# Kernel tuning notes

Measured on AMD Instinct MI355X. Metric: run time of the kernel, lower is better.

Reference implementation:

```python
import jax, jax.numpy as jnp
import numpy as np

N, D = 4096, 512
W_L2, W_TOPO = 1.0, 1.0
BIG = jnp.float32(1e30)


def setup_inputs() -> dict:
    key = jax.random.key(0)
    k1, k2 = jax.random.split(key)
    x_1 = jax.random.normal(k1, (N, D), dtype=jnp.float32)
    x_2 = jax.random.normal(k2, (N, D), dtype=jnp.float32)
    return {"x_1": x_1, "x_2": x_2}


def _pdist(x):
    # Euclidean pairwise distances [n, n]; diagonal set to BIG so it is never
    # selected as an MST edge and sqrt(0) never appears in the grad path.
    sq = jnp.sum(x * x, axis=1)
    d2 = sq[:, None] + sq[None, :] - 2.0 * (x @ x.T)
    d2 = jnp.maximum(d2, 1e-12)
    n = x.shape[0]
    d2 = jnp.where(jnp.eye(n, dtype=bool), BIG, d2)
    return jnp.sqrt(d2)


def _h0_deaths(dist):
    # H0 persistence of the Vietoris-Rips filtration == MST edge weights
    # (births are all 0). Prim's algorithm via lax.scan, O(n^2).
    n = dist.shape[0]
    in_tree0 = jnp.zeros(n, dtype=bool).at[0].set(True)

    def step(carry, _):
        min_dist, in_tree = carry  # min_dist[k] = min edge from tree to k
        md = jnp.where(in_tree, BIG, min_dist)
        j = jnp.argmin(md)
        w = md[j]  # weight of the MST edge added this step = an H0 death
        min_dist = jnp.minimum(min_dist, dist[j])
        in_tree = in_tree.at[j].set(True)
        return (min_dist, in_tree), w

    (_, _), deaths = jax.lax.scan(step, (dist[0], in_tree0), None, length=n - 1)
    return deaths  # [n-1]


def _wasserstein1(d1, d2):
    # 1-Wasserstein between two H0 diagrams {(0, death_i)} with L_inf ground
    # metric and diagonal projections allowed. Equal-cardinality diagrams on
    # the birth=0 axis: match sorted deaths, per-pair cost is the cheaper of
    # direct matching |a-b| or routing both points to the diagonal (a+b)/2.
    a = jnp.sort(d1)
    b = jnp.sort(d2)
    cost = jnp.minimum(jnp.abs(a - b), 0.5 * (a + b))
    return jnp.sum(cost)


def reference(x_1, x_2):
    representation_loss = jnp.mean((x_1 - x_2) ** 2)
    deaths_1 = _h0_deaths(_pdist(x_1))
    deaths_2 = _h0_deaths(_pdist(x_2))
    topological_loss = _wasserstein1(deaths_1, deaths_2)
    return W_L2 * representation_loss + W_TOPO * topological_loss
```

## Files before the change

kernel.cpp:

```cpp
#include <hip/hip_runtime.h>

#define N 4096
#define D 512
#define BIG 1e30f
#define CMAX 2048
#define CMAX2 1024
#define NW (N / 32)

typedef unsigned long long u64;
typedef unsigned short u16;
typedef _Float16 f16x8 __attribute__((ext_vector_type(8)));
typedef float floatx4 __attribute__((ext_vector_type(4)));

__global__ __launch_bounds__(256) void prep_kernel(const float* __restrict__ x1,
                                                   const float* __restrict__ x2,
                                                   u16* __restrict__ h1,
                                                   u16* __restrict__ h2,
                                                   float* __restrict__ sq,
                                                   float* __restrict__ accumArr,
                                                   int* __restrict__ comp,
                                                   u64* __restrict__ compBest,
                                                   int* __restrict__ comp_c,
                                                   int* __restrict__ doneFlag) {
    const int tid = blockIdx.x * 256 + threadIdx.x;
    if (tid < 2 * N) {
        comp[tid] = tid & (N - 1);
        compBest[tid] = ~0ull;
    }
    if (tid < 2 * CMAX) comp_c[tid] = tid & (CMAX - 1);
    if (tid == 0) doneFlag[0] = 0;

    const int wave = threadIdx.x >> 6, lane = threadIdx.x & 63;
    const int row = blockIdx.x * 4 + wave;
    const float4* r1 = (const float4*)(x1 + (size_t)row * D);
    const float4* r2 = (const float4*)(x2 + (size_t)row * D);
    float4 a0 = r1[lane * 2], a1 = r1[lane * 2 + 1];
    float4 b0 = r2[lane * 2], b1 = r2[lane * 2 + 1];
    ushort4* o1 = (ushort4*)(h1 + (size_t)row * D + lane * 8);
    ushort4* o2 = (ushort4*)(h2 + (size_t)row * D + lane * 8);
    o1[0] = make_ushort4(__builtin_bit_cast(u16, (_Float16)a0.x), __builtin_bit_cast(u16, (_Float16)a0.y),
                         __builtin_bit_cast(u16, (_Float16)a0.z), __builtin_bit_cast(u16, (_Float16)a0.w));
    o1[1] = make_ushort4(__builtin_bit_cast(u16, (_Float16)a1.x), __builtin_bit_cast(u16, (_Float16)a1.y),
                         __builtin_bit_cast(u16, (_Float16)a1.z), __builtin_bit_cast(u16, (_Float16)a1.w));
    o2[0] = make_ushort4(__builtin_bit_cast(u16, (_Float16)b0.x), __builtin_bit_cast(u16, (_Float16)b0.y),
                         __builtin_bit_cast(u16, (_Float16)b0.z), __builtin_bit_cast(u16, (_Float16)b0.w));
    o2[1] = make_ushort4(__builtin_bit_cast(u16, (_Float16)b1.x), __builtin_bit_cast(u16, (_Float16)b1.y),
                         __builtin_bit_cast(u16, (_Float16)b1.z), __builtin_bit_cast(u16, (_Float16)b1.w));
    float s1 = 0.f, s2 = 0.f, sr = 0.f;
    float av[8] = {a0.x, a0.y, a0.z, a0.w, a1.x, a1.y, a1.z, a1.w};
    float bv[8] = {b0.x, b0.y, b0.z, b0.w, b1.x, b1.y, b1.z, b1.w};
#pragma unroll
    for (int e = 0; e < 8; ++e) {
        s1 = fmaf(av[e], av[e], s1);
        s2 = fmaf(bv[e], bv[e], s2);
        float d = av[e] - bv[e];
        sr = fmaf(d, d, sr);
    }
#pragma unroll
    for (int off = 32; off > 0; off >>= 1) {
        s1 += __shfl_down(s1, off, 64);
        s2 += __shfl_down(s2, off, 64);
        sr += __shfl_down(sr, off, 64);
    }
    __shared__ float wsr[4];
    if (lane == 0) {
        sq[row] = s1;
        sq[N + row] = s2;
        wsr[wave] = sr;
    }
    __syncthreads();
    if (threadIdx.x == 0)
        accumArr[blockIdx.x] = wsr[0] + wsr[1] + wsr[2] + wsr[3];
}

#define BM 128
#define BN 128
#define BK 32
#define NB (N / BM)
#define NPAIR (NB * (NB + 1) / 2)
#define NT (D / BK)

__global__ __launch_bounds__(256) void gemm_dist_sym_kernel(const u16* __restrict__ h1,
                                                            const u16* __restrict__ h2,
                                                            const float* __restrict__ sqn,
                                                            float* __restrict__ dist1,
                                                            float* __restrict__ dist2,
                                                            u64* __restrict__ compBest) {
    const int m = blockIdx.z;
    const u16* H = m ? h2 : h1;
    const float* SQ = sqn + (size_t)m * N;
    float* dist = m ? dist2 : dist1;
    u64* cb = compBest + (size_t)m * N;

    const int t = blockIdx.x;
    int by = (int)((65.0f - sqrtf(4225.0f - 8.0f * (float)t)) * 0.5f);
    while (by > 0 && by * 32 - by * (by - 1) / 2 > t) --by;
    while ((by + 1) * 32 - (by + 1) * by / 2 <= t) ++by;
    const int bx = by + (t - (by * 32 - by * (by - 1) / 2));
    const bool diag = (by == bx);

    __shared__ u16 SH[4 * BM * BK];
    u16* A0 = SH;
    u16* B0 = SH + BM * BK;
    u16* A1 = SH + 2 * BM * BK;
    u16* B1 = SH + 3 * BM * BK;

    const int tid = threadIdx.x;
    const int wave = tid >> 6, lane = tid & 63;
    const int wm = wave >> 1, wn = wave & 1;
    const int row0 = by * BM, col0 = bx * BN;

    floatx4 acc[4][4] = {};

    const int srow = lane >> 2;
    const int scol = (lane & 3) * 8;

#define STAGE(AB, BB, K0)                                                                      \
    {                                                                                          \
        _Pragma("unroll") for (int i_ = 0; i_ < 2; ++i_) {                                     \
            const int rb_ = wave * 32 + i_ * 16;                                               \
            const u16* ga_ = H + (size_t)(row0 + rb_ + srow) * D + (K0) + scol;                \
            __builtin_amdgcn_global_load_lds(                                                  \
                (const __attribute__((address_space(1))) unsigned int*)ga_,                    \
                (__attribute__((address_space(3))) unsigned int*)&(AB)[rb_ * BK], 16, 0, 0);   \
            if (!diag) {                                                                       \
                const u16* gb_ = H + (size_t)(col0 + rb_ + srow) * D + (K0) + scol;            \
                __builtin_amdgcn_global_load_lds(                                              \
                    (const __attribute__((address_space(1))) unsigned int*)gb_,                \
                    (__attribute__((address_space(3))) unsigned int*)&(BB)[rb_ * BK], 16, 0, 0); \
            }                                                                                  \
        }                                                                                      \
    }

    STAGE(A0, B0, 0);
    __syncthreads();

    const int fo = (lane >> 4) * 8;
    const int fm = lane & 15;
#pragma unroll 2
    for (int kt = 0; kt < NT; ++kt) {
        u16* Ac = (kt & 1) ? A1 : A0;
        u16* Bc = (kt & 1) ? B1 : B0;
        if (kt + 1 < NT) {
            u16* An = (kt & 1) ? A0 : A1;
            u16* Bn = (kt & 1) ? B0 : B1;
            STAGE(An, Bn, (kt + 1) * BK);
        }
        const u16* Bs = diag ? Ac : Bc;
        f16x8 a8[4], b8[4];
#pragma unroll
        for (int s = 0; s < 4; ++s) {
            a8[s] = *(const f16x8*)&Ac[(wm * 64 + s * 16 + fm) * BK + fo];
            b8[s] = *(const f16x8*)&Bs[(wn * 64 + s * 16 + fm) * BK + fo];
        }
#pragma unroll
        for (int i = 0; i < 4; ++i)
#pragma unroll
            for (int j = 0; j < 4; ++j)
                acc[i][j] = __builtin_amdgcn_mfma_f32_16x16x32_f16(a8[i], b8[j], acc[i][j], 0, 0, 0);
        __syncthreads();
    }
#undef STAGE

    float* Cs = (float*)SH + wave * 1024;

    const int lr = lane & 15;
    const int lq = lane >> 4;
    float sc[4];
#pragma unroll
    for (int ns = 0; ns < 4; ++ns) sc[ns] = SQ[col0 + wn * 64 + ns * 16 + lr];
    u64 colBest[4] = {~0ull, ~0ull, ~0ull, ~0ull};
#pragma unroll
    for (int ms = 0; ms < 4; ++ms) {
        const int rb = row0 + wm * 64 + ms * 16 + lq * 4;
        float srow_[4];
#pragma unroll
        for (int r = 0; r < 4; ++r) srow_[r] = SQ[rb + r];
#pragma unroll
        for (int r = 0; r < 4; ++r) {
            const int row = rb + r;
            float dval[4];
#pragma unroll
            for (int ns = 0; ns < 4; ++ns) {
                const int col = col0 + wn * 64 + ns * 16 + lr;
                float d2 = srow_[r] + sc[ns] - 2.0f * acc[ms][ns][r];
                dval[ns] = (row == col) ? BIG : sqrtf(fmaxf(d2, 1e-12f));
            }
            float vmin = fminf(fminf(dval[0], dval[1]), fminf(dval[2], dval[3]));
            int nsel = (dval[0] == vmin) ? 0 : (dval[1] == vmin) ? 1 : (dval[2] == vmin) ? 2 : 3;
            u64 pmin = (((u64)__float_as_uint(vmin)) << 32) | (unsigned)(col0 + wn * 64 + nsel * 16 + lr);
#pragma unroll
            for (int msk = 1; msk < 16; msk <<= 1) {
                u64 o = __shfl_xor(pmin, msk, 64);
                pmin = o < pmin ? o : pmin;
            }
            if (lr == 0) atomicMin(&cb[row], pmin);
            if (!diag) {
#pragma unroll
                for (int ns = 0; ns < 4; ++ns) {
                    u64 p = (((u64)__float_as_uint(dval[ns])) << 32) | (unsigned)row;
                    colBest[ns] = p < colBest[ns] ? p : colBest[ns];
                }
            }
#pragma unroll
            for (int ns = 0; ns < 4; ++ns)
                Cs[(lq * 4 + r) * 64 + ns * 16 + lr] = dval[ns];
        }
#pragma unroll
        for (int p = 0; p < 4; ++p) {
            float4 v4 = *(float4*)&Cs[p * 256 + lane * 4];
            const int gr = row0 + wm * 64 + ms * 16 + p * 4 + (lane >> 4);
            const int gc = col0 + wn * 64 + (lane & 15) * 4;
            *(float4*)&dist[(size_t)gr * N + gc] = v4;
        }
    }
    if (!diag) {
#pragma unroll
        for (int ns = 0; ns < 4; ++ns) {
            u64 b = colBest[ns];
            u64 o = __shfl_xor(b, 16, 64);
            b = o < b ? o : b;
            o = __shfl_xor(b, 32, 64);
            b = o < b ? o : b;
            if (lq == 0) atomicMin(&cb[col0 + wn * 64 + ns * 16 + lr], b);
        }
    }
}

__global__ __launch_bounds__(1024) void merge1i_kernel(int* __restrict__ comp,
                                                       u64* __restrict__ compBest,
                                                       float* __restrict__ deaths,
                                                       int* __restrict__ cnt,
                                                       int* __restrict__ numComp,
                                                       int* __restrict__ numC1,
                                                       unsigned* __restrict__ distc_u) {
    const int t = threadIdx.x;
    if (blockIdx.x >= 2) {
        const size_t idx = (size_t)(blockIdx.x - 2) * 1024 + t;
        uint4 v = make_uint4(0x7f800000u, 0x7f800000u, 0x7f800000u, 0x7f800000u);
        ((uint4*)distc_u)[idx] = v;
        ((uint4*)distc_u)[idx + 1048576] = v;
        return;
    }
    const int m = blockIdx.x;
    int* cp = comp + (size_t)m * N;
    u64* cb = compBest + (size_t)m * N;
    float* dth = deaths + (size_t)m * N;

    __shared__ int pa[N];
    __shared__ int pb[N];
    __shared__ unsigned flagbits[NW];
    __shared__ int wpc[NW];
    __shared__ int done;

    if (t == 0) cnt[m] = 0;
    __syncthreads();

    for (int c = t; c < N; c += 1024) {
        u64 best = cb[c];
        int p = c;
        if (best != ~0ull) {
            int j = (int)(unsigned)best;
            int c2 = cp[j];
            u64 best2 = cb[c2];
            int j2 = (int)(unsigned)best2;
            bool mutual = (cp[j2] == c);
            if (!(mutual && c < c2)) {
                p = c2;
                int idx = atomicAdd(cnt + m, 1);
                dth[idx] = __uint_as_float((unsigned)(best >> 32));
            }
        }
        pa[c] = p;
    }

    int* A = pa;
    int* B = pb;
    while (true) {
        __syncthreads();
        if (t == 0) done = 1;
        __syncthreads();
        bool ch = false;
        for (int c = t; c < N; c += 1024) {
            int g = A[A[c]];
            B[c] = g;
            ch |= (g != A[c]);
        }
        if (ch) done = 0;
        __syncthreads();
        int* tmp = A; A = B; B = tmp;
        if (done) break;
    }

    for (int w = t; w < NW; w += 1024) flagbits[w] = 0u;
    __syncthreads();
    for (int i = t; i < N; i += 1024)
        atomicOr(&flagbits[A[i] >> 5], 1u << (A[i] & 31));
    __syncthreads();
    if (t < NW) wpc[t] = __popc(flagbits[t]);
    __syncthreads();
    for (int off = 1; off < NW; off <<= 1) {
        int v = 0;
        if (t < NW) v = wpc[t] + ((t >= off) ? wpc[t - off] : 0);
        __syncthreads();
        if (t < NW) wpc[t] = v;
        __syncthreads();
    }
    for (int i = t; i < N; i += 1024) {
        int root = A[i];
        int w = root >> 5, b = root & 31;
        int base = w ? wpc[w - 1] : 0;
        unsigned mask = b ? ((1u << b) - 1u) : 0u;
        cp[i] = base + __popc(flagbits[w] & mask);
    }
    for (int c = t; c < N; c += 1024) cb[c] = ~0ull;
    if (t == 0) {
        int C1 = wpc[NW - 1];
        numC1[m] = C1;
        numComp[m] = C1;
    }
}

__global__ __launch_bounds__(256) void rowatomic_kernel(const float* __restrict__ dist1,
                                                        const float* __restrict__ dist2,
                                                        const int* __restrict__ comp,
                                                        unsigned* __restrict__ distc_u) {
    const int m = blockIdx.y;
    const float* dist = m ? dist2 : dist1;
    const int* cp = comp + (size_t)m * N;
    const int i = blockIdx.x;
    const float4* row4 = (const float4*)(dist + (size_t)i * N);
    const int4* cp4 = (const int4*)cp;
    __shared__ unsigned bins[CMAX];
    const int t = threadIdx.x;
    for (int b = t; b < CMAX; b += 256) bins[b] = 0x7f800000u;
    __syncthreads();
    const int q0 = (i >> 7) << 5;
    for (int q = q0 + t; q < N / 4; q += 256) {
        float4 v = row4[q];
        int4 cj = cp4[q];
        atomicMin(&bins[cj.x], __float_as_uint(v.x));
        atomicMin(&bins[cj.y], __float_as_uint(v.y));
        atomicMin(&bins[cj.z], __float_as_uint(v.z));
        atomicMin(&bins[cj.w], __float_as_uint(v.w));
    }
    __syncthreads();
    unsigned* drow = distc_u + ((size_t)m * CMAX + cp[i]) * CMAX;
    for (int b = t; b < CMAX; b += 256) {
        unsigned v = bins[b];
        if (v != 0x7f800000u) atomicMin(&drow[b], v);
    }
}

#define CT 64
#define NCT (CMAX / CT)
#define NPAIRC (NCT * (NCT + 1) / 2)
__global__ __launch_bounds__(256) void symscan_kernel(unsigned* __restrict__ distc_u,
                                                      u64* __restrict__ compBest,
                                                      const int* __restrict__ numComp,
                                                      const int* __restrict__ numC1,
                                                      unsigned* __restrict__ distc2_u) {
    const int tid = threadIdx.x;
    if (blockIdx.x >= NPAIRC) {
        const size_t base = ((size_t)blockIdx.y * 256 + (blockIdx.x - NPAIRC)) * 256 + tid;
        uint4 v = make_uint4(0x7f800000u, 0x7f800000u, 0x7f800000u, 0x7f800000u);
#pragma unroll
        for (int k = 0; k < 4; ++k)
            ((uint4*)distc2_u)[base + (size_t)k * 131072] = v;
        return;
    }
    const int m = blockIdx.y;
    if (numComp[m] <= 1) return;
    const int C1 = numC1[m];
    const int t = blockIdx.x;
    int a = (int)((65.0f - sqrtf(4225.0f - 8.0f * (float)t)) * 0.5f);
    while (a > 0 && a * 32 - a * (a - 1) / 2 > t) --a;
    while ((a + 1) * 32 - (a + 1) * a / 2 <= t) ++a;
    const int b = a + (t - (a * 32 - a * (a - 1) / 2));
    if (a * CT >= C1 || b * CT >= C1) return;

    unsigned* Dm = distc_u + (size_t)m * CMAX * CMAX;
    unsigned* P = Dm + (size_t)(a * CT) * CMAX + b * CT;
    unsigned* Q = Dm + (size_t)(b * CT) * CMAX + a * CT;
    u64* cb = compBest + (size_t)m * N;

    __shared__ float L[CT][CT + 1];
    __shared__ float M[CT][CT + 1];
#pragma unroll
    for (int e0 = 0; e0 < 4; ++e0) {
        int e = e0 * 256 + tid;
        int r = e >> 4, c4 = (e & 15) << 2;
        float4 v = *(const float4*)&Q[(size_t)r * CMAX + c4];
        L[r][c4] = v.x; L[r][c4 + 1] = v.y; L[r][c4 + 2] = v.z; L[r][c4 + 3] = v.w;
    }
    __syncthreads();
#pragma unroll
    for (int e0 = 0; e0 < 4; ++e0) {
        int e = e0 * 256 + tid;
        int r = e >> 4, c4 = (e & 15) << 2;
        float4 v = *(const float4*)&P[(size_t)r * CMAX + c4];
        float4 f;
        f.x = fminf(v.x, L[c4 + 0][r]);
        f.y = fminf(v.y, L[c4 + 1][r]);
        f.z = fminf(v.z, L[c4 + 2][r]);
        f.w = fminf(v.w, L[c4 + 3][r]);
        *(float4*)&P[(size_t)r * CMAX + c4] = f;
        M[r][c4] = f.x; M[r][c4 + 1] = f.y; M[r][c4 + 2] = f.z; M[r][c4 + 3] = f.w;
    }
    __syncthreads();

    {
        const int rloc = tid >> 2;
        const int r = a * CT + rloc;
        const int c0 = (tid & 3) * 16;
        u64 best = ~0ull;
#pragma unroll
        for (int c = 0; c < 16; ++c) {
            const int j = b * CT + c0 + c;
            const unsigned bits = __float_as_uint(M[rloc][c0 + c]);
            if (j < C1 && j != r && bits < 0x7f800000u) {
                u64 p = (((u64)bits) << 32) | (unsigned)j;
                best = p < best ? p : best;
            }
        }
        u64 o = __shfl_xor(best, 1, 64); best = o < best ? o : best;
        o = __shfl_xor(best, 2, 64); best = o < best ? o : best;
        if ((tid & 3) == 0 && r < C1 && best != ~0ull) atomicMin(&cb[r], best);
    }

    if (a == b) return;

    {
        const int rloc = tid >> 2;
        const int r = b * CT + rloc;
        const int c0 = (tid & 3) * 16;
        u64 best = ~0ull;
#pragma unroll
        for (int c = 0; c < 16; ++c) {
            const int j = a * CT + c0 + c;
            const unsigned bits = __float_as_uint(M[c0 + c][rloc]);
            if (j < C1 && bits < 0x7f800000u) {
                u64 p = (((u64)bits) << 32) | (unsigned)j;
                best = p < best ? p : best;
            }
        }
        u64 o = __shfl_xor(best, 1, 64); best = o < best ? o : best;
        o = __shfl_xor(best, 2, 64); best = o < best ? o : best;
        if ((tid & 3) == 0 && r < C1 && best != ~0ull) atomicMin(&cb[r], best);
    }

#pragma unroll
    for (int e0 = 0; e0 < 4; ++e0) {
        int e = e0 * 256 + tid;
        int r = e >> 4, c4 = (e & 15) << 2;
        float4 f;
        f.x = M[c4 + 0][r];
        f.y = M[c4 + 1][r];
        f.z = M[c4 + 2][r];
        f.w = M[c4 + 3][r];
        *(float4*)&Q[(size_t)r * CMAX + c4] = f;
    }
}

__global__ __launch_bounds__(1024) void merge2_kernel(int* __restrict__ comp_c,
                                                      u64* __restrict__ compBest,
                                                      float* __restrict__ deaths,
                                                      int* __restrict__ cnt,
                                                      int* __restrict__ numComp,
                                                      const int* __restrict__ numC1,
                                                      int* __restrict__ numC2,
                                                      int* __restrict__ comp_c2) {
    const int m = blockIdx.x;
    const int t = threadIdx.x;
    const int C1 = numC1[m];
    int* cc2i = comp_c2 + (size_t)m * CMAX2;
    for (int c = t; c < CMAX2; c += 1024) cc2i[c] = c;
    if (numComp[m] <= 1) {
        if (t == 0) numC2[m] = numComp[m];
        return;
    }
    int* cc = comp_c + (size_t)m * CMAX;
    u64* cb = compBest + (size_t)m * N;
    float* dth = deaths + (size_t)m * N;

    __shared__ int pa[CMAX];
    __shared__ int pb[CMAX];
    __shared__ unsigned flagbits[CMAX / 32];
    __shared__ int wpc[CMAX / 32];
    __shared__ int done;

    for (int c = t; c < C1; c += 1024) {
        u64 best = cb[c];
        int p = c;
        if (best != ~0ull) {
            int j = (int)(unsigned)best;
            int c2 = cc[j];
            u64 best2 = cb[c2];
            int j2 = (int)(unsigned)best2;
            bool mutual = (cc[j2] == c);
            if (!(mutual && c < c2)) {
                p = c2;
                int idx = atomicAdd(cnt + m, 1);
                dth[idx] = __uint_as_float((unsigned)(best >> 32));
            }
        }
        pa[c] = p;
    }

    int* A = pa;
    int* B = pb;
    while (true) {
        __syncthreads();
        if (t == 0) done = 1;
        __syncthreads();
        bool ch = false;
        for (int c = t; c < C1; c += 1024) {
            int g = A[A[c]];
            B[c] = g;
            ch |= (g != A[c]);
        }
        if (ch) done = 0;
        __syncthreads();
        int* tmp = A; A = B; B = tmp;
        if (done) break;
    }

    for (int w = t; w < CMAX / 32; w += 1024) flagbits[w] = 0u;
    __syncthreads();
    for (int j = t; j < C1; j += 1024)
        atomicOr(&flagbits[A[j] >> 5], 1u << (A[j] & 31));
    __syncthreads();
    if (t < CMAX / 32) wpc[t] = __popc(flagbits[t]);
    __syncthreads();
    for (int off = 1; off < CMAX / 32; off <<= 1) {
        int v = 0;
        if (t < CMAX / 32) v = wpc[t] + ((t >= off) ? wpc[t - off] : 0);
        __syncthreads();
        if (t < CMAX / 32) wpc[t] = v;
        __syncthreads();
    }
    for (int j = t; j < C1; j += 1024) {
        int root = A[j];
        int w = root >> 5, b = root & 31;
        int base = w ? wpc[w - 1] : 0;
        unsigned mask = b ? ((1u << b) - 1u) : 0u;
        cc[j] = base + __popc(flagbits[w] & mask);
    }
    for (int c = t; c < C1; c += 1024) cb[c] = ~0ull;
    if (t == 0) {
        int C2 = wpc[CMAX / 32 - 1];
        numC2[m] = C2;
        numComp[m] = C2;
    }
}

__global__ __launch_bounds__(256) void rowatomic2_kernel(const float* __restrict__ distc,
                                                         const int* __restrict__ comp_c,
                                                         const int* __restrict__ numComp,
                                                         const int* __restrict__ numC1,
                                                         unsigned* __restrict__ distc2_u) {
    const int m = blockIdx.y;
    if (numComp[m] <= 1) return;
    const int C1 = numC1[m];
    const int r = blockIdx.x;
    if (r >= C1) return;
    const int* cc = comp_c + (size_t)m * CMAX;
    const float* row = distc + ((size_t)m * CMAX + r) * CMAX;
    __shared__ unsigned bins[CMAX2];
    const int t = threadIdx.x;
    for (int b = t; b < CMAX2; b += 256) bins[b] = 0x7f800000u;
    __syncthreads();
    for (int j = t; j < C1; j += 256)
        atomicMin(&bins[cc[j]], __float_as_uint(row[j]));
    __syncthreads();
    unsigned* drow = distc2_u + ((size_t)m * CMAX2 + cc[r]) * CMAX2;
    for (int b = t; b < CMAX2; b += 256) {
        unsigned v = bins[b];
        if (v != 0x7f800000u) atomicMin(&drow[b], v);
    }
}

__global__ __launch_bounds__(1024) void finish_kernel(const float* __restrict__ distc2,
                                                      const int* __restrict__ comp_c2,
                                                      float* __restrict__ deaths,
                                                      int* __restrict__ cnt,
                                                      int* __restrict__ numComp,
                                                      const int* __restrict__ numC2,
                                                      const float* __restrict__ accumArr,
                                                      int* __restrict__ doneFlag,
                                                      float* __restrict__ out) {
    const int m = blockIdx.x;
    int nc = numComp[m];
    const int C2 = numC2[m];
    const float* Dm = distc2 + (size_t)m * CMAX2 * CMAX2;
    float* dth = deaths + (size_t)m * N;
    const int t = threadIdx.x;
    const int wave = t >> 6, lane = t & 63;
    __shared__ int comp[CMAX2];
    __shared__ u64 cb[CMAX2];
    __shared__ int pa[CMAX2];
    __shared__ int pb[CMAX2];
    __shared__ unsigned flags[CMAX2 / 32];
    __shared__ int done, ncs, lastf;
    __shared__ float s[N];
    __shared__ float wsum[16];
    __shared__ float rsum[16];

    if (nc > 1) {
        for (int c = t; c < C2; c += 1024) {
            comp[c] = comp_c2[(size_t)m * CMAX2 + c];
            cb[c] = ~0ull;
        }
        __syncthreads();

        for (int round = 0; round < 10 && nc > 1; ++round) {
            for (int r = wave; r < C2; r += 16) {
                const int myc = comp[r];
                const float* row = Dm + (size_t)r * CMAX2;
                u64 best = ~0ull;
                for (int j = lane; j < C2; j += 64) {
                    if (comp[j] != myc) {
                        u64 p = (((u64)__float_as_uint(row[j])) << 32) | (unsigned)j;
                        best = p < best ? p : best;
                    }
                }
#pragma unroll
                for (int off = 32; off > 0; off >>= 1) {
                    u64 o = __shfl_down(best, off, 64);
                    best = o < best ? o : best;
                }
                if (lane == 0) atomicMin(&cb[myc], best);
            }
            __syncthreads();
            for (int c = t; c < C2; c += 1024) {
                u64 best = cb[c];
                int p = c;
                if (best != ~0ull) {
                    int j = (int)(unsigned)best;
                    int c2 = comp[j];
                    u64 best2 = cb[c2];
                    int j2 = (int)(unsigned)best2;
                    bool mutual = (comp[j2] == c);
                    if (!(mutual && c < c2)) {
                        p = c2;
                        int idx = atomicAdd(cnt + m, 1);
                        dth[idx] = __uint_as_float((unsigned)(best >> 32));
                    }
                }
                pa[c] = p;
            }
            int* A = pa; int* B = pb;
            while (true) {
                __syncthreads();
                if (t == 0) done = 1;
                __syncthreads();
                bool ch = false;
                for (int c = t; c < C2; c += 1024) {
                    int g = A[A[c]];
                    B[c] = g;
                    ch |= (g != A[c]);
                }
                if (ch) done = 0;
                __syncthreads();
                int* tmp = A; A = B; B = tmp;
                if (done) break;
            }
            for (int w = t; w < CMAX2 / 32; w += 1024) flags[w] = 0u;
            __syncthreads();
            for (int j = t; j < C2; j += 1024) {
                int root = A[comp[j]];
                comp[j] = root;
                atomicOr(&flags[root >> 5], 1u << (root & 31));
            }
            for (int c = t; c < C2; c += 1024) cb[c] = ~0ull;
            __syncthreads();
            if (t == 0) {
                int sacc = 0;
                for (int w = 0; w < CMAX2 / 32; ++w) sacc += __popc(flags[w]);
                ncs = sacc;
            }
            __syncthreads();
            nc = ncs;
        }
        if (t == 0) numComp[m] = nc;
    }
    __syncthreads();

    for (int i = t; i < N; i += 1024)
        s[i] = (i < N - 1) ? dth[i] : BIG;
    __syncthreads();
    for (int k = 2; k <= N; k <<= 1) {
        for (int jj = k >> 1; jj > 0; jj >>= 1) {
            for (int i = t; i < N; i += 1024) {
                int ixj = i ^ jj;
                if (ixj > i) {
                    float a = s[i], b = s[ixj];
                    bool up = ((i & k) == 0);
                    bool sw = up ? (a > b) : (a < b);
                    if (sw) { s[i] = b; s[ixj] = a; }
                }
            }
            __syncthreads();
        }
    }
    for (int i = t; i < N; i += 1024) dth[i] = s[i];

    __threadfence();
    __syncthreads();
    if (t == 0) lastf = (atomicAdd(doneFlag, 1) == 1) ? 1 : 0;
    __syncthreads();
    if (!lastf) return;
    __threadfence();
    const float* s1 = deaths;
    const float* s2 = deaths + N;
    float sum = 0.f;
    for (int i = t; i < N - 1; i += 1024) {
        float a = s1[i], b = s2[i];
        sum += fminf(fabsf(a - b), 0.5f * (a + b));
    }
    float ra = accumArr[t];
#pragma unroll
    for (int off = 32; off > 0; off >>= 1) {
        sum += __shfl_down(sum, off, 64);
        ra += __shfl_down(ra, off, 64);
    }
    if (lane == 0) { wsum[wave] = sum; rsum[wave] = ra; }
    __syncthreads();
    if (t == 0) {
        float tot = 0.f, rt = 0.f;
        for (int k = 0; k < 16; ++k) { tot += wsum[k]; rt += rsum[k]; }
        out[0] = rt * (1.0f / ((float)N * (float)D)) + tot;
    }
}

extern "C" void kernel_launch(void* const* d_in, const int* in_sizes, int n_in,
                              void* d_out, int out_size, void* d_ws, size_t ws_size,
                              hipStream_t stream) {
    const float* x1 = (const float*)d_in[0];
    const float* x2 = (const float*)d_in[1];
    float* out = (float*)d_out;
    float* ws = (float*)d_ws;

    const size_t nn = (size_t)N * N;
    const size_t cc2 = (size_t)CMAX * CMAX;

    float* dist1 = ws;
    float* dist2 = ws + nn;
    float* distc = ws + 2 * nn;
    u16* h1 = (u16*)distc;
    u16* h2 = h1 + (size_t)N * D;
    u64* compBest = (u64*)(distc + 2 * cc2);
    int* comp      = (int*)(compBest + 2 * N);
    int* comp_c    = comp + 2 * N;
    float* deaths  = (float*)(comp_c + 2 * CMAX);
    int* cnt       = (int*)(deaths + 2 * N);
    int* numComp   = cnt + 2;
    int* numC1     = numComp + 2;
    int* numC2     = numC1 + 2;
    int* doneFlag  = numC2 + 2;
    float* sq      = (float*)(doneFlag + 2);
    float* accumArr = sq + 2 * N;
    float* distc2  = dist1;
    int* comp_c2   = (int*)(distc2 + 2 * (size_t)CMAX2 * CMAX2);

    prep_kernel<<<N / 4, 256, 0, stream>>>(x1, x2, h1, h2, sq, accumArr, comp, compBest,
                                           comp_c, doneFlag);
    gemm_dist_sym_kernel<<<dim3(NPAIR, 1, 2), 256, 0, stream>>>(h1, h2, sq, dist1, dist2, compBest);
    merge1i_kernel<<<2 + 1024, 1024, 0, stream>>>(comp, compBest, deaths, cnt, numComp, numC1,
                                                  (unsigned*)distc);
    rowatomic_kernel<<<dim3(N, 2), 256, 0, stream>>>(dist1, dist2, comp, (unsigned*)distc);
    symscan_kernel<<<dim3(NPAIRC + 256, 2), 256, 0, stream>>>((unsigned*)distc, compBest,
                                                              numComp, numC1, (unsigned*)distc2);
    merge2_kernel<<<2, 1024, 0, stream>>>(comp_c, compBest, deaths, cnt, numComp, numC1, numC2,
                                          comp_c2);
    rowatomic2_kernel<<<dim3(CMAX, 2), 256, 0, stream>>>(distc, comp_c, numComp, numC1,
                                                         (unsigned*)distc2);
    finish_kernel<<<2, 1024, 0, stream>>>(distc2, comp_c2, deaths, cnt, numComp, numC2,
                                          accumArr, doneFlag, out);
}
```

Before: 251.9 us.

## Add grid-wide third Boruvka contraction level and register-resident bitonic sort

Adds a third Boruvka level that runs on the whole grid. scan3 finds each component's cheapest outgoing edge, merge3 merges components and relabels them compactly, and rowatomic3 contracts the distance matrix to at most 512 components. Only a much smaller matrix is left for the single-block finish kernel, whose serial rounds over a 1024-wide matrix were a bottleneck on two blocks. The finish-stage bitonic sort now keeps four values per thread in registers and uses wave shuffles for small strides, which avoids shared-memory traffic and many barriers. The cost is three more kernel launches, and the code assumes the component count after level three fits in 512.

After: 227.8 us. 9.6% less time.

```diff
diff --git a/kernel.cpp b/kernel.cpp
--- a/kernel.cpp
+++ b/kernel.cpp
@@ -5,6 +5,7 @@
 #define BIG 1e30f
 #define CMAX 2048
 #define CMAX2 1024
+#define CMAX3 512
 #define NW (N / 32)
 
 typedef unsigned long long u64;
@@ -580,45 +581,201 @@
     }
 }
 
-__global__ __launch_bounds__(1024) void finish_kernel(const float* __restrict__ distc2,
-                                                      const int* __restrict__ comp_c2,
+__global__ __launch_bounds__(256) void scan3_kernel(const float* __restrict__ distc2,
+                                                    const int* __restrict__ comp_c2,
+                                                    u64* __restrict__ compBest,
+                                                    const int* __restrict__ numComp,
+                                                    const int* __restrict__ numC2,
+                                                    unsigned* __restrict__ distc3_u) {
+    const int t = threadIdx.x;
+    if (blockIdx.x >= 2 * CMAX2) {
+        const size_t idx = (size_t)(blockIdx.x - 2 * CMAX2) * 256 + t;
+        uint4 v = make_uint4(0x7f800000u, 0x7f800000u, 0x7f800000u, 0x7f800000u);
+        ((uint4*)distc3_u)[idx] = v;
+        ((uint4*)distc3_u)[idx + 65536] = v;
+        return;
+    }
+    const int m = blockIdx.x >> 10;
+    if (numComp[m] <= 1) return;
+    const int C2 = numC2[m];
+    const int r = blockIdx.x & (CMAX2 - 1);
+    if (r >= C2) return;
+    const int* cc = comp_c2 + (size_t)m * CMAX2;
+    u64* cb = compBest + (size_t)m * N;
+    const int myc = cc[r];
+    const float4* row4 = (const float4*)(distc2 + ((size_t)m * CMAX2 + r) * CMAX2);
+    const int4* cc4 = (const int4*)cc;
+    float4 v = row4[t];
+    int4 cj = cc4[t];
+    int j0 = t * 4;
+    u64 p0 = (j0 + 0 < C2 && cj.x != myc) ? ((((u64)__float_as_uint(v.x)) << 32) | (unsigned)(j0 + 0)) : ~0ull;
+    u64 p1 = (j0 + 1 < C2 && cj.y != myc) ? ((((u64)__float_as_uint(v.y)) << 32) | (unsigned)(j0 + 1)) : ~0ull;
+    u64 p2 = (j0 + 2 < C2 && cj.z != myc) ? ((((u64)__float_as_uint(v.z)) << 32) | (unsigned)(j0 + 2)) : ~0ull;
+    u64 p3 = (j0 + 3 < C2 && cj.w != myc) ? ((((u64)__float_as_uint(v.w)) << 32) | (unsigned)(j0 + 3)) : ~0ull;
+    u64 q0 = p0 < p1 ? p0 : p1;
+    u64 q1 = p2 < p3 ? p2 : p3;
+    u64 best = q0 < q1 ? q0 : q1;
+#pragma unroll
+    for (int off = 32; off > 0; off >>= 1) {
+        u64 o = __shfl_down(best, off, 64);
+        best = o < best ? o : best;
+    }
+    if ((t & 63) == 0) atomicMin(cb + myc, best);
+}
+
+__global__ __launch_bounds__(1024) void merge3_kernel(int* __restrict__ comp_c2,
+                                                      u64* __restrict__ compBest,
                                                       float* __restrict__ deaths,
                                                       int* __restrict__ cnt,
                                                       int* __restrict__ numComp,
                                                       const int* __restrict__ numC2,
+                                                      int* __restrict__ numC3) {
+    const int m = blockIdx.x;
+    const int t = threadIdx.x;
+    if (numComp[m] <= 1) {
+        if (t == 0) numC3[m] = numComp[m];
+        return;
+    }
+    const int C2 = numC2[m];
+    int* cc = comp_c2 + (size_t)m * CMAX2;
+    u64* cb = compBest + (size_t)m * N;
+    float* dth = deaths + (size_t)m * N;
+
+    __shared__ int pa[CMAX2];
+    __shared__ int pb[CMAX2];
+    __shared__ unsigned flagbits[CMAX2 / 32];
+    __shared__ int wpc[CMAX2 / 32];
+    __shared__ int done;
+
+    for (int c = t; c < C2; c += 1024) {
+        u64 best = cb[c];
+        int p = c;
+        if (best != ~0ull) {
+            int j = (int)(unsigned)best;
+            int c2 = cc[j];
+            u64 best2 = cb[c2];
+            int j2 = (int)(unsigned)best2;
+            bool mutual = (cc[j2] == c);
+            if (!(mutual && c < c2)) {
+                p = c2;
+                int idx = atomicAdd(cnt + m, 1);
+                dth[idx] = __uint_as_float((unsigned)(best >> 32));
+            }
+        }
+        pa[c] = p;
+    }
+
+    int* A = pa;
+    int* B = pb;
+    while (true) {
+        __syncthreads();
+        if (t == 0) done = 1;
+        __syncthreads();
+        bool ch = false;
+        for (int c = t; c < C2; c += 1024) {
+            int g = A[A[c]];
+            B[c] = g;
+            ch |= (g != A[c]);
+        }
+        if (ch) done = 0;
+        __syncthreads();
+        int* tmp = A; A = B; B = tmp;
+        if (done) break;
+    }
+
+    for (int w = t; w < CMAX2 / 32; w += 1024) flagbits[w] = 0u;
+    __syncthreads();
+    for (int j = t; j < C2; j += 1024)
+        atomicOr(&flagbits[A[j] >> 5], 1u << (A[j] & 31));
+    __syncthreads();
+    if (t < CMAX2 / 32) wpc[t] = __popc(flagbits[t]);
+    __syncthreads();
+    for (int off = 1; off < CMAX2 / 32; off <<= 1) {
+        int v = 0;
+        if (t < CMAX2 / 32) v = wpc[t] + ((t >= off) ? wpc[t - off] : 0);
+        __syncthreads();
+        if (t < CMAX2 / 32) wpc[t] = v;
+        __syncthreads();
+    }
+    for (int j = t; j < C2; j += 1024) {
+        int root = A[j];
+        int w = root >> 5, b = root & 31;
+        int base = w ? wpc[w - 1] : 0;
+        unsigned mask = b ? ((1u << b) - 1u) : 0u;
+        cc[j] = base + __popc(flagbits[w] & mask);
+    }
+    for (int c = t; c < C2; c += 1024) cb[c] = ~0ull;
+    if (t == 0) {
+        int C3 = wpc[CMAX2 / 32 - 1];
+        numC3[m] = C3;
+        numComp[m] = C3;
+    }
+}
+
+__global__ __launch_bounds__(256) void rowatomic3_kernel(const float* __restrict__ distc2,
+                                                         const int* __restrict__ comp_c2,
+                                                         const int* __restrict__ numComp,
+                                                         const int* __restrict__ numC2,
+                                                         unsigned* __restrict__ distc3_u) {
+    const int m = blockIdx.y;
+    if (numComp[m] <= 1) return;
+    const int C2 = numC2[m];
+    const int r = blockIdx.x;
+    if (r >= C2) return;
+    const int* cc = comp_c2 + (size_t)m * CMAX2;
+    const float* row = distc2 + ((size_t)m * CMAX2 + r) * CMAX2;
+    __shared__ unsigned bins[CMAX3];
+    const int t = threadIdx.x;
+    for (int b = t; b < CMAX3; b += 256) bins[b] = 0x7f800000u;
+    __syncthreads();
+    for (int j = t; j < C2; j += 256)
+        atomicMin(&bins[cc[j]], __float_as_uint(row[j]));
+    __syncthreads();
+    unsigned* drow = distc3_u + ((size_t)m * CMAX3 + cc[r]) * CMAX3;
+    for (int b = t; b < CMAX3; b += 256) {
+        unsigned v = bins[b];
+        if (v != 0x7f800000u) atomicMin(&drow[b], v);
+    }
+}
+
+__global__ __launch_bounds__(1024) void finish_kernel(const float* __restrict__ distc3,
+                                                      float* __restrict__ deaths,
+                                                      int* __restrict__ cnt,
+                                                      int* __restrict__ numComp,
+                                                      const int* __restrict__ numC3,
                                                       const float* __restrict__ accumArr,
                                                       int* __restrict__ doneFlag,
                                                       float* __restrict__ out) {
     const int m = blockIdx.x;
     int nc = numComp[m];
-    const int C2 = numC2[m];
-    const float* Dm = distc2 + (size_t)m * CMAX2 * CMAX2;
+    const int C3 = numC3[m];
+    const float* Dm = distc3 + (size_t)m * CMAX3 * CMAX3;
     float* dth = deaths + (size_t)m * N;
     const int t = threadIdx.x;
     const int wave = t >> 6, lane = t & 63;
-    __shared__ int comp[CMAX2];
-    __shared__ u64 cb[CMAX2];
-    __shared__ int pa[CMAX2];
-    __shared__ int pb[CMAX2];
-    __shared__ unsigned flags[CMAX2 / 32];
+    __shared__ int comp[CMAX3];
+    __shared__ u64 cb[CMAX3];
+    __shared__ int pa[CMAX3];
+    __shared__ int pb[CMAX3];
+    __shared__ unsigned flags[CMAX3 / 32];
     __shared__ int done, ncs, lastf;
     __shared__ float s[N];
     __shared__ float wsum[16];
     __shared__ float rsum[16];
 
     if (nc > 1) {
-        for (int c = t; c < C2; c += 1024) {
-            comp[c] = comp_c2[(size_t)m * CMAX2 + c];
+        for (int c = t; c < C3; c += 1024) {
+            comp[c] = c;
             cb[c] = ~0ull;
         }
         __syncthreads();
 
         for (int round = 0; round < 10 && nc > 1; ++round) {
-            for (int r = wave; r < C2; r += 16) {
+            for (int r = wave; r < C3; r += 16) {
                 const int myc = comp[r];
-                const float* row = Dm + (size_t)r * CMAX2;
+                const float* row = Dm + (size_t)r * CMAX3;
                 u64 best = ~0ull;
-                for (int j = lane; j < C2; j += 64) {
+                for (int j = lane; j < C3; j += 64) {
                     if (comp[j] != myc) {
                         u64 p = (((u64)__float_as_uint(row[j])) << 32) | (unsigned)j;
                         best = p < best ? p : best;
@@ -632,7 +789,7 @@
                 if (lane == 0) atomicMin(&cb[myc], best);
             }
             __syncthreads();
-            for (int c = t; c < C2; c += 1024) {
+            for (int c = t; c < C3; c += 1024) {
                 u64 best = cb[c];
                 int p = c;
                 if (best != ~0ull) {
@@ -655,7 +812,7 @@
                 if (t == 0) done = 1;
                 __syncthreads();
                 bool ch = false;
-                for (int c = t; c < C2; c += 1024) {
+                for (int c = t; c < C3; c += 1024) {
                     int g = A[A[c]];
                     B[c] = g;
                     ch |= (g != A[c]);
@@ -665,18 +822,18 @@
                 int* tmp = A; A = B; B = tmp;
                 if (done) break;
             }
-            for (int w = t; w < CMAX2 / 32; w += 1024) flags[w] = 0u;
+            for (int w = t; w < CMAX3 / 32; w += 1024) flags[w] = 0u;
             __syncthreads();
-            for (int j = t; j < C2; j += 1024) {
+            for (int j = t; j < C3; j += 1024) {
                 int root = A[comp[j]];
                 comp[j] = root;
                 atomicOr(&flags[root >> 5], 1u << (root & 31));
             }
-            for (int c = t; c < C2; c += 1024) cb[c] = ~0ull;
+            for (int c = t; c < C3; c += 1024) cb[c] = ~0ull;
             __syncthreads();
             if (t == 0) {
                 int sacc = 0;
-                for (int w = 0; w < CMAX2 / 32; ++w) sacc += __popc(flags[w]);
+                for (int w = 0; w < CMAX3 / 32; ++w) sacc += __popc(flags[w]);
                 ncs = sacc;
             }
             __syncthreads();
@@ -686,24 +843,61 @@
     }
     __syncthreads();
 
-    for (int i = t; i < N; i += 1024)
-        s[i] = (i < N - 1) ? dth[i] : BIG;
-    __syncthreads();
+    const int t4 = t << 2;
+    float v0, v1, v2, v3;
+    {
+        float4 l4 = *(const float4*)&dth[t4];
+        v0 = l4.x; v1 = l4.y; v2 = l4.z; v3 = l4.w;
+        if (t == 1023) v3 = BIG;
+    }
+#define CSWAP(a, b, up)                         \
+    {                                           \
+        float mn_ = fminf(a, b), mx_ = fmaxf(a, b); \
+        a = (up) ? mn_ : mx_;                   \
+        b = (up) ? mx_ : mn_;                   \
+    }
     for (int k = 2; k <= N; k <<= 1) {
         for (int jj = k >> 1; jj > 0; jj >>= 1) {
-            for (int i = t; i < N; i += 1024) {
-                int ixj = i ^ jj;
-                if (ixj > i) {
-                    float a = s[i], b = s[ixj];
-                    bool up = ((i & k) == 0);
-                    bool sw = up ? (a > b) : (a < b);
-                    if (sw) { s[i] = b; s[ixj] = a; }
-                }
-            }
-            __syncthreads();
-        }
-    }
-    for (int i = t; i < N; i += 1024) dth[i] = s[i];
+            if (jj >= 256) {
+                s[t4] = v0; s[t4 + 1] = v1; s[t4 + 2] = v2; s[t4 + 3] = v3;
+                __syncthreads();
+                const bool up = ((t4 & k) == 0);
+                const bool lower = ((t4 & jj) == 0);
+                const bool mk = (up == lower);
+                float o0 = s[t4 ^ jj], o1 = s[(t4 + 1) ^ jj];
+                float o2 = s[(t4 + 2) ^ jj], o3 = s[(t4 + 3) ^ jj];
+                v0 = mk ? fminf(v0, o0) : fmaxf(v0, o0);
+                v1 = mk ? fminf(v1, o1) : fmaxf(v1, o1);
+                v2 = mk ? fminf(v2, o2) : fmaxf(v2, o2);
+                v3 = mk ? fminf(v3, o3) : fmaxf(v3, o3);
+                __syncthreads();
+            } else if (jj >= 4) {
+                const int sl = jj >> 2;
+                const bool up = ((t4 & k) == 0);
+                const bool lower = ((lane & sl) == 0);
+                const bool mk = (up == lower);
+                float o0 = __shfl_xor(v0, sl, 64);
+                float o1 = __shfl_xor(v1, sl, 64);
+                float o2 = __shfl_xor(v2, sl, 64);
+                float o3 = __shfl_xor(v3, sl, 64);
+                v0 = mk ? fminf(v0, o0) : fmaxf(v0, o0);
+                v1 = mk ? fminf(v1, o1) : fmaxf(v1, o1);
+                v2 = mk ? fminf(v2, o2) : fmaxf(v2, o2);
+                v3 = mk ? fminf(v3, o3) : fmaxf(v3, o3);
+            } else if (jj == 2) {
+                const bool up = ((t4 & k) == 0);
+                CSWAP(v0, v2, up);
+                CSWAP(v1, v3, up);
+            } else {
+                const bool u01 = ((t4 & k) == 0);
+                const bool u23 = (((t4 + 2) & k) == 0);
+                CSWAP(v0, v1, u01);
+                CSWAP(v2, v3, u23);
+            }
+        }
+    }
+#undef CSWAP
+    *(float4*)&dth[t4] = make_float4(v0, v1, v2, v3);
 
     __threadfence();
     __syncthreads();
@@ -757,11 +951,13 @@
     int* numComp   = cnt + 2;
     int* numC1     = numComp + 2;
     int* numC2     = numC1 + 2;
-    int* doneFlag  = numC2 + 2;
+    int* numC3     = numC2 + 2;
+    int* doneFlag  = numC3 + 2;
     float* sq      = (float*)(doneFlag + 2);
     float* accumArr = sq + 2 * N;
     float* distc2  = dist1;
     int* comp_c2   = (int*)(distc2 + 2 * (size_t)CMAX2 * CMAX2);
+    float* distc3  = distc;
 
     prep_kernel<<<N / 4, 256, 0, stream>>>(x1, x2, h1, h2, sq, accumArr, comp, compBest,
                                            comp_c, doneFlag);
@@ -775,6 +971,11 @@
                                           comp_c2);
     rowatomic2_kernel<<<dim3(CMAX, 2), 256, 0, stream>>>(distc, comp_c, numComp, numC1,
                                                          (unsigned*)distc2);
-    finish_kernel<<<2, 1024, 0, stream>>>(distc2, comp_c2, deaths, cnt, numComp, numC2,
+    scan3_kernel<<<2 * CMAX2 + 256, 256, 0, stream>>>(distc2, comp_c2, compBest, numComp, numC2,
+                                                      (unsigned*)distc3);
+    merge3_kernel<<<2, 1024, 0, stream>>>(comp_c2, compBest, deaths, cnt, numComp, numC2, numC3);
+    rowatomic3_kernel<<<dim3(CMAX2, 2), 256, 0, stream>>>(distc2, comp_c2, numComp, numC2,
+                                                          (unsigned*)distc3);
+    finish_kernel<<<2, 1024, 0, stream>>>(distc3, deaths, cnt, numComp, numC3,
                                           accumArr, doneFlag, out);
 }
```
